# Kernel optimization log

Hardware: AMD Instinct MI355X
Metric: run time of the kernel (lower is better)

Reference implementation:

```python
import jax, jax.numpy as jnp
import numpy as np

H, DH = 16, 64          # num_heads, dim_head
DIM = 1024              # dim_ltn
EPS = 1e-5


def setup_inputs() -> dict:
    key = jax.random.key(0)
    ks = jax.random.split(key, 8)
    b, n_txt, t, m = 2, 2048, 4, 256
    text = jax.random.normal(ks[0], (b, n_txt, DIM), dtype=jnp.float32)
    image = jax.random.normal(ks[1], (b, t, m, DIM), dtype=jnp.float32)
    locations = jax.random.randint(ks[2], (b, n_txt), 0, 2)  # 0/1 media markers
    s = DIM ** -0.5
    Wq = jax.random.normal(ks[3], (DIM, H * DH), dtype=jnp.float32) * s
    Wkv = jax.random.normal(ks[4], (DIM, 2 * H * DH), dtype=jnp.float32) * s
    Wo = jax.random.normal(ks[5], (H * DH, DIM), dtype=jnp.float32) * s
    ln_gamma = jnp.ones((DIM,), dtype=jnp.float32)
    ln_beta = jnp.zeros((DIM,), dtype=jnp.float32)
    return {"text": text, "image": image, "locations": locations,
            "Wq": Wq, "Wkv": Wkv, "Wo": Wo,
            "ln_gamma": ln_gamma, "ln_beta": ln_beta}


def reference(text, image, locations, Wq, Wkv, Wo, ln_gamma, ln_beta):
    scale = DH ** -0.5
    b, t, m, d = image.shape
    # LayerNorm(text)
    mu = text.mean(-1, keepdims=True)
    var = ((text - mu) ** 2).mean(-1, keepdims=True)
    tn = (text - mu) / jnp.sqrt(var + EPS) * ln_gamma + ln_beta
    img = image.reshape(b, t * m, d)             # b (t m) d
    q = tn @ Wq                                  # b n (h dh)
    k, v = jnp.split(img @ Wkv, 2, axis=-1)      # each b tm (h dh)
    split_heads = lambda x: x.reshape(x.shape[0], x.shape[1], H, DH).transpose(0, 2, 1, 3)
    q, k, v = split_heads(q), split_heads(k), split_heads(v)
    attn = jnp.einsum('bhid,bhjd->bhij', q, k) * scale   # b h n (t m)
    txt_time = jnp.cumsum(locations, axis=-1)            # b n : media index per text token
    viz_time = jnp.repeat(jnp.arange(1, t + 1), m)       # (t m)
    # only_attend_to_immediate -> equality mask
    mask = txt_time[:, None, :, None] == viz_time[None, None, None, :]
    neg = -jnp.finfo(attn.dtype).max
    attn = jnp.where(mask, attn, neg)
    attn = jax.nn.softmax(attn, axis=-1)
    # zero attention for text tokens before any media (txt_time == 0)
    attn = jnp.where((txt_time == 0)[:, None, :, None], 0.0, attn)
    out = jnp.einsum('bhij,bhjd->bhid', attn, v)
    out = out.transpose(0, 2, 1, 3).reshape(b, -1, H * DH)
    return out @ Wo
```

## Files before the change

kernel.cpp:

```cpp
#include <hip/hip_runtime.h>

#define BATCH 2
#define NTXT  2048
#define TMED  4
#define MMED  256
#define TM    (TMED * MMED)
#define DIM   1024
#define NH    16
#define DHD   64
#define KVW   2048
#define RMAX  256
#define QSTR  ((size_t)BATCH * RMAX * DIM)

typedef _Float16 f16x8 __attribute__((ext_vector_type(8)));
typedef float    f32x4 __attribute__((ext_vector_type(4)));

__global__ __launch_bounds__(256) void k1_prep(
    const int* __restrict__ loc, const float* __restrict__ Wkv,
    int* __restrict__ tt, int* __restrict__ seg, float* __restrict__ vbar,
    _Float16* __restrict__ WkvT) {
  __shared__ float tile[64][65];
  __shared__ int tots[256];
  __shared__ int s_start, s_end;
  const int bid = blockIdx.x;
  const int tid = threadIdx.x;
  if (bid < BATCH) {
    const int b = bid;
    if (tid == 0) { s_start = NTXT; s_end = NTXT; }
    __syncthreads();
    int v[8];
    int run = 0;
    const int base = b * NTXT + tid * 8;
#pragma unroll
    for (int k = 0; k < 8; k++) { run += loc[base + k]; v[k] = run; }
    tots[tid] = run; __syncthreads();
    for (int off = 1; off < 256; off <<= 1) {
      const int add = (tid >= off) ? tots[tid - off] : 0;
      __syncthreads();
      tots[tid] += add;
      __syncthreads();
    }
    const int excl = tots[tid] - run;
#pragma unroll
    for (int k = 0; k < 8; k++) {
      const int tv = excl + v[k];
      tt[base + k] = tv;
      if (tv >= 1) atomicMin(&s_start, tid * 8 + k);
      if (tv >= 5) atomicMin(&s_end, tid * 8 + k);
    }
    __syncthreads();
    if (tid == 0) {
      seg[b * 2]     = s_start;
      seg[b * 2 + 1] = s_end - s_start;
    }
  } else if (bid == 2) {
    for (int c = tid; c < 2 * BATCH * DIM; c += 256) vbar[c] = 0.f;
  } else {
    const int idx = bid - 3;
    const int k0 = (idx & 15) * 64, n0 = (idx >> 4) * 64;
    const int r = tid >> 4, c4 = (tid & 15) * 4;
#pragma unroll
    for (int i = 0; i < 4; i++) {
      const float4 v = *reinterpret_cast<const float4*>(
          Wkv + (size_t)(k0 + r + i * 16) * KVW + n0 + c4);
      tile[r + i * 16][c4 + 0] = v.x; tile[r + i * 16][c4 + 1] = v.y;
      tile[r + i * 16][c4 + 2] = v.z; tile[r + i * 16][c4 + 3] = v.w;
    }
    __syncthreads();
#pragma unroll
    for (int it = 0; it < 2; it++) {
      const int chunk = it * 256 + tid;
      const int n = chunk >> 3, kc = (chunk & 7) * 8;
      f16x8 h;
#pragma unroll
      for (int j = 0; j < 8; j++) h[j] = (_Float16)tile[kc + j][n];
      *reinterpret_cast<f16x8*>(WkvT + (size_t)(n0 + n) * DIM + k0 + kc) = h;
    }
  }
}

__global__ __launch_bounds__(256) void k2_gemm_qproj(
    const float* __restrict__ image, const _Float16* __restrict__ WkvT,
    const float* __restrict__ text, const float* __restrict__ Wq,
    const float* __restrict__ gamma, const float* __restrict__ beta,
    const int* __restrict__ seg, _Float16* __restrict__ kv16,
    float* __restrict__ qpart, float* __restrict__ vbar) {
  __shared__ char smem[8192];
  const int idx = blockIdx.x;
  const int tid = threadIdx.x;
  if (idx >= 64) {
    _Float16* As = (_Float16*)smem;
    _Float16* Bs = As + 64 * 32;
    const int gid = idx - 64;
    const int lane = tid & 63, wid = tid >> 6;
    const int wm = wid & 1, wn = wid >> 1;
    const int row0 = (gid >> 5) * 64, col0 = (gid & 31) * 64;
    const int srow = tid >> 2, skc = (tid & 3) * 8;
    const int frow = lane & 15, fq = lane >> 4;
    f32x4 acc[2][2] = {};
    for (int k0 = 0; k0 < DIM; k0 += 32) {
      const float* ap = image + (size_t)(row0 + srow) * DIM + k0 + skc;
      const float4 a0 = *reinterpret_cast<const float4*>(ap);
      const float4 a1 = *reinterpret_cast<const float4*>(ap + 4);
      f16x8 av;
      av[0] = (_Float16)a0.x; av[1] = (_Float16)a0.y;
      av[2] = (_Float16)a0.z; av[3] = (_Float16)a0.w;
      av[4] = (_Float16)a1.x; av[5] = (_Float16)a1.y;
      av[6] = (_Float16)a1.z; av[7] = (_Float16)a1.w;
      const f16x8 bv = *reinterpret_cast<const f16x8*>(
          WkvT + (size_t)(col0 + srow) * DIM + k0 + skc);
      __syncthreads();
      *reinterpret_cast<f16x8*>(As + tid * 8) = av;
      *reinterpret_cast<f16x8*>(Bs + tid * 8) = bv;
      __syncthreads();
      f16x8 af[2], bf[2];
#pragma unroll
      for (int mt = 0; mt < 2; mt++)
        af[mt] = *reinterpret_cast<const f16x8*>(
            As + (wm * 32 + mt * 16 + frow) * 32 + fq * 8);
#pragma unroll
      for (int nt = 0; nt < 2; nt++)
        bf[nt] = *reinterpret_cast<const f16x8*>(
            Bs + (wn * 32 + nt * 16 + frow) * 32 + fq * 8);
#pragma unroll
      for (int mt = 0; mt < 2; mt++)
#pragma unroll
        for (int nt = 0; nt < 2; nt++)
          acc[mt][nt] = __builtin_amdgcn_mfma_f32_16x16x32_f16(
              af[mt], bf[nt], acc[mt][nt], 0, 0, 0);
    }
#pragma unroll
    for (int mt = 0; mt < 2; mt++)
#pragma unroll
      for (int nt = 0; nt < 2; nt++) {
        const int col = col0 + wn * 32 + nt * 16 + frow;
#pragma unroll
        for (int r = 0; r < 4; r++) {
          const int row = row0 + wm * 32 + mt * 16 + fq * 4 + r;
          kv16[(size_t)row * KVW + col] = (_Float16)acc[mt][nt][r];
        }
      }
    if (col0 >= DIM) {
      const int b = row0 >> 10;
#pragma unroll
      for (int nt = 0; nt < 2; nt++) {
        float s = 0.f;
#pragma unroll
        for (int mt = 0; mt < 2; mt++)
#pragma unroll
          for (int r = 0; r < 4; r++) s += acc[mt][nt][r];
        s += __shfl_down(s, 32);
        s += __shfl_down(s, 16);
        if (lane < 16)
          atomicAdd(&vbar[b * DIM + (col0 - DIM) + wn * 32 + nt * 16 + lane],
                    s * (1.0f / (float)TM));
      }
    }
  } else {
    float* tn_s = (float*)smem;
    const int j = idx;
    const int b = j >> 5, nt = (j >> 2) & 7, cc = j & 3;
    const int n0 = nt * 128, c0 = cc * 256;
    const int lane = tid & 63, w = tid >> 6;
    const int n = tid & 127, rh = tid >> 7;
    const int i0 = seg[b * 2];
    const int cnt = min(seg[b * 2 + 1], RMAX);
    float* qp = qpart + (size_t)cc * QSTR;
    for (int r0 = 0; r0 < cnt; r0 += 4) {
      const int rows = min(4, cnt - r0);
      if (w < rows) {
        const float* xrow = text + (size_t)(b * NTXT + i0 + r0 + w) * DIM;
        float s = 0.f, sq = 0.f;
#pragma unroll
        for (int u = 0; u < 16; u++) {
          const float x = xrow[lane + 64 * u];
          s += x; sq += x * x;
        }
#pragma unroll
        for (int off = 32; off > 0; off >>= 1) {
          s += __shfl_xor(s, off);
          sq += __shfl_xor(sq, off);
        }
        const float mu = s * (1.0f / DIM);
        const float rstd = rsqrtf(sq * (1.0f / DIM) - mu * mu + 1e-5f);
#pragma unroll
        for (int u = 0; u < 4; u++) {
          const int c = c0 + lane + 64 * u;
          tn_s[w * 256 + lane + 64 * u] =
              (xrow[c] - mu) * rstd * gamma[c] + beta[c];
        }
      }
      __syncthreads();
      float a0 = 0.f, a1 = 0.f;
      for (int c = 0; c < 256; c++) {
        const float wv = Wq[(size_t)(c0 + c) * DIM + n0 + n];
        a0 += tn_s[(rh * 2) * 256 + c] * wv;
        a1 += tn_s[(rh * 2 + 1) * 256 + c] * wv;
      }
      if (rh * 2 < rows)
        qp[(size_t)(b * RMAX + r0 + rh * 2) * DIM + n0 + n] = a0;
      if (rh * 2 + 1 < rows)
        qp[(size_t)(b * RMAX + r0 + rh * 2 + 1) * DIM + n0 + n] = a1;
      __syncthreads();
    }
  }
}

__global__ __launch_bounds__(512) void k3_obar(
    const float* __restrict__ vbar, const float* __restrict__ Wo,
    float* __restrict__ obar) {
  __shared__ float vb_s[128];
  const int bid = blockIdx.x;
  const int tid = threadIdx.x;
  const int b = bid >> 4, et = (bid >> 3) & 1, cc = bid & 7;
  const int e = et * 512 + tid, c0 = cc * 128;
  if (tid < 128) vb_s[tid] = vbar[b * DIM + c0 + tid];
  __syncthreads();
  float s = 0.f;
  for (int c = 0; c < 128; c++)
    s += vb_s[c] * Wo[(size_t)(c0 + c) * DIM + e];
  atomicAdd(&obar[b * DIM + e], s);
}

__global__ __launch_bounds__(256) void k4_fill_attn(
    const float* __restrict__ text, const _Float16* __restrict__ kv16,
    const float* __restrict__ Wq, const float* __restrict__ Wo,
    const float* __restrict__ gamma, const float* __restrict__ beta,
    const int* __restrict__ tt, const int* __restrict__ seg,
    const float* __restrict__ obar, const float* __restrict__ qpart,
    float* __restrict__ oacc, float* __restrict__ out) {
  __shared__ float red[256];
  __shared__ float pbuf[256];
  const int idx = blockIdx.x;
  const int tid = threadIdx.x;
  if (idx < BATCH * NTXT) {
    const int b = idx >> 11;
    const int i = idx & (NTXT - 1);
    const int t = tt[idx];
    float* orow = out + (size_t)idx * DIM;
    if (t == 0) {
      *reinterpret_cast<float4*>(&orow[tid * 4]) =
          make_float4(0.f, 0.f, 0.f, 0.f);
      return;
    }
    if (t > TMED) {
      *reinterpret_cast<float4*>(&orow[tid * 4]) =
          *reinterpret_cast<const float4*>(&obar[b * DIM + tid * 4]);
      return;
    }
    if (i - seg[b * 2] < RMAX) return;
    __shared__ float tns[DIM];
    __shared__ float qrow[DIM];
    __shared__ float oaccs[DIM];
    const float* xrow = text + (size_t)idx * DIM;
    float x[4];
    float s = 0.f;
#pragma unroll
    for (int u = 0; u < 4; u++) { x[u] = xrow[tid + 256 * u]; s += x[u]; }
    red[tid] = s; __syncthreads();
    for (int st = 128; st > 0; st >>= 1) {
      if (tid < st) red[tid] += red[tid + st];
      __syncthreads();
    }
    const float mu = red[0] * (1.0f / DIM); __syncthreads();
    float vs = 0.f;
#pragma unroll
    for (int u = 0; u < 4; u++) { float d = x[u] - mu; vs += d * d; }
    red[tid] = vs; __syncthreads();
    for (int st = 128; st > 0; st >>= 1) {
      if (tid < st) red[tid] += red[tid + st];
      __syncthreads();
    }
    const float rstd = rsqrtf(red[0] * (1.0f / DIM) + 1e-5f); __syncthreads();
#pragma unroll
    for (int u = 0; u < 4; u++) {
      const int c = tid + 256 * u;
      tns[c] = (x[u] - mu) * rstd * gamma[c] + beta[c];
    }
    __syncthreads();
    {
      float qa[4] = {0.f, 0.f, 0.f, 0.f};
      for (int c = 0; c < DIM; c++) {
        const float tv = tns[c];
        const float* wp = Wq + (size_t)c * DIM + tid;
#pragma unroll
        for (int u = 0; u < 4; u++) qa[u] += tv * wp[256 * u];
      }
#pragma unroll
      for (int u = 0; u < 4; u++) qrow[tid + 256 * u] = qa[u];
    }
    __syncthreads();
    const size_t kvrow0 = (size_t)(b * TM + (t - 1) * MMED) * KVW;
    const int d0 = tid & 63, g = tid >> 6;
    for (int h = 0; h < NH; h++) {
      const _Float16* krow = kv16 + kvrow0 + (size_t)tid * KVW + h * DHD;
      float sc = 0.f;
#pragma unroll
      for (int d = 0; d < DHD; d++) sc += qrow[h * DHD + d] * (float)krow[d];
      sc *= 0.125f;
      red[tid] = sc; __syncthreads();
      for (int st = 128; st > 0; st >>= 1) {
        if (tid < st) red[tid] = fmaxf(red[tid], red[tid + st]);
        __syncthreads();
      }
      const float mx = red[0]; __syncthreads();
      const float e = __expf(sc - mx);
      red[tid] = e; __syncthreads();
      for (int st = 128; st > 0; st >>= 1) {
        if (tid < st) red[tid] += red[tid + st];
        __syncthreads();
      }
      const float inv = 1.0f / red[0]; __syncthreads();
      pbuf[tid] = e * inv; __syncthreads();
      const _Float16* vbase =
          kv16 + kvrow0 + (size_t)(g * 64) * KVW + DIM + h * DHD + d0;
      float a = 0.f;
#pragma unroll 8
      for (int jj = 0; jj < 64; jj++)
        a += pbuf[g * 64 + jj] * (float)vbase[(size_t)jj * KVW];
      red[tid] = a; __syncthreads();
      if (tid < 64)
        oaccs[h * DHD + tid] =
            red[tid] + red[64 + tid] + red[128 + tid] + red[192 + tid];
      __syncthreads();
    }
    float oa[4] = {0.f, 0.f, 0.f, 0.f};
    for (int c = 0; c < DIM; c++) {
      const float ov = oaccs[c];
      const float* wp = Wo + (size_t)c * DIM + tid;
#pragma unroll
      for (int u = 0; u < 4; u++) oa[u] += ov * wp[256 * u];
    }
#pragma unroll
    for (int u = 0; u < 4; u++) orow[tid + 256 * u] = oa[u];
  } else {
    __shared__ float qs[DHD];
    const int j = idx - BATCH * NTXT;
    const int h = j & 15, rt = (j >> 4) & 31, b = j >> 9;
    const int i0 = seg[b * 2];
    const int cnt = min(seg[b * 2 + 1], RMAX);
    const int d0 = tid & 63, g = tid >> 6;
    for (int r = rt; r < cnt; r += 32) {
      const int i = i0 + r;
      const int t = tt[b * NTXT + i];
      if (tid < 64) {
        const size_t qoff = (size_t)(b * RMAX + r) * DIM + h * DHD + tid;
        qs[tid] = qpart[qoff] + qpart[QSTR + qoff] +
                  qpart[2 * QSTR + qoff] + qpart[3 * QSTR + qoff];
      }
      __syncthreads();
      const size_t kvrow0 = (size_t)(b * TM + (t - 1) * MMED) * KVW;
      const _Float16* krow = kv16 + kvrow0 + (size_t)tid * KVW + h * DHD;
      float sc = 0.f;
#pragma unroll
      for (int d = 0; d < DHD; d += 8) {
        const f16x8 kk = *reinterpret_cast<const f16x8*>(krow + d);
#pragma unroll
        for (int u = 0; u < 8; u++) sc += qs[d + u] * (float)kk[u];
      }
      sc *= 0.125f;
      red[tid] = sc; __syncthreads();
      for (int st = 128; st > 0; st >>= 1) {
        if (tid < st) red[tid] = fmaxf(red[tid], red[tid + st]);
        __syncthreads();
      }
      const float mx = red[0]; __syncthreads();
      const float e = __expf(sc - mx);
      red[tid] = e; __syncthreads();
      for (int st = 128; st > 0; st >>= 1) {
        if (tid < st) red[tid] += red[tid + st];
        __syncthreads();
      }
      const float inv = 1.0f / red[0]; __syncthreads();
      pbuf[tid] = e * inv; __syncthreads();
      const _Float16* vbase =
          kv16 + kvrow0 + (size_t)(g * 64) * KVW + DIM + h * DHD + d0;
      float a = 0.f;
#pragma unroll 8
      for (int jj = 0; jj < 64; jj++)
        a += pbuf[g * 64 + jj] * (float)vbase[(size_t)jj * KVW];
      red[tid] = a; __syncthreads();
      if (tid < 64)
        oacc[(size_t)(b * RMAX + r) * DIM + h * DHD + tid] =
            red[tid] + red[64 + tid] + red[128 + tid] + red[192 + tid];
      __syncthreads();
    }
  }
}

__global__ __launch_bounds__(256) void k5_oproj(
    const float* __restrict__ oacc, const float* __restrict__ Wo,
    const int* __restrict__ seg, float* __restrict__ out) {
  const int ct = blockIdx.x;
  const int rt = blockIdx.y;
  const int b = blockIdx.z;
  const int i0 = seg[b * 2];
  const int cnt = min(seg[b * 2 + 1], RMAX);
  const int tid = threadIdx.x;
  const int d0 = tid & 63, g = tid >> 6;
  __shared__ float op[4][64];
  for (int r = rt; r < cnt; r += 32) {
    const float* arow = oacc + (size_t)(b * RMAX + r) * DIM;
    const float* wo = Wo + (size_t)(g * 256) * DIM + ct * 64 + d0;
    float s = 0.f;
    for (int c = 0; c < 256; c++) s += arow[g * 256 + c] * wo[(size_t)c * DIM];
    op[g][d0] = s; __syncthreads();
    if (tid < 64)
      out[(size_t)(b * NTXT + i0 + r) * DIM + ct * 64 + tid] =
          op[0][tid] + op[1][tid] + op[2][tid] + op[3][tid];
    __syncthreads();
  }
}

extern "C" void kernel_launch(void* const* d_in, const int* in_sizes, int n_in,
                              void* d_out, int out_size, void* d_ws, size_t ws_size,
                              hipStream_t stream) {
  const float* text  = (const float*)d_in[0];
  const float* image = (const float*)d_in[1];
  const int*   loc   = (const int*)d_in[2];
  const float* Wq    = (const float*)d_in[3];
  const float* Wkv   = (const float*)d_in[4];
  const float* Wo    = (const float*)d_in[5];
  const float* gamma = (const float*)d_in[6];
  const float* beta  = (const float*)d_in[7];
  float* out = (float*)d_out;

  _Float16* kv16  = (_Float16*)d_ws;
  _Float16* WkvT  = kv16 + (size_t)BATCH * TM * KVW;
  float*    oacc  = (float*)WkvT;
  float*    qpart = (float*)(WkvT + (size_t)KVW * DIM);
  float*    vbar  = qpart + 4 * QSTR;
  float*    obar  = vbar + BATCH * DIM;
  int*      tt    = (int*)(obar + BATCH * DIM);
  int*      seg   = tt + BATCH * NTXT;

  k1_prep<<<515, 256, 0, stream>>>(loc, Wkv, tt, seg, vbar, WkvT);
  k2_gemm_qproj<<<1088, 256, 0, stream>>>(image, WkvT, text, Wq, gamma, beta,
                                          seg, kv16, qpart, vbar);
  k3_obar<<<32, 512, 0, stream>>>(vbar, Wo, obar);
  k4_fill_attn<<<BATCH * NTXT + NH * 32 * BATCH, 256, 0, stream>>>(
      text, kv16, Wq, Wo, gamma, beta, tt, seg, obar, qpart, oacc, out);
  k5_oproj<<<dim3(16, 32, BATCH), 256, 0, stream>>>(oacc, Wo, seg, out);
}
```

Before: 187.2 us.

## Compute vbar from image mean, enlarge KV GEMM tile, restage attention and oproj

The mean of V is now computed algebraically as mean(image) @ Wv in the prep kernel, written as deterministic partial sums instead of atomics from the GEMM epilogue. The obar projection moves into the GEMM kernel as partials. The KV GEMM tile grows from 64 to 128 rows per block, which halves the number of blocks and reuses each B tile across more rows. Attention moves into its own kernel together with the obar reduction, and the output projection runs alongside the fill kernel, which removes one launch. The cost is extra partial-buffer traffic, and the fp32 mean path differs numerically from the previous f16 accumulation.

```diff
diff --git a/kernel.cpp b/kernel.cpp
--- a/kernel.cpp
+++ b/kernel.cpp
@@ -11,14 +11,16 @@
 #define KVW   2048
 #define RMAX  256
 #define QSTR  ((size_t)BATCH * RMAX * DIM)
+#define BD    (BATCH * DIM)
 
 typedef _Float16 f16x8 __attribute__((ext_vector_type(8)));
 typedef float    f32x4 __attribute__((ext_vector_type(4)));
 
 __global__ __launch_bounds__(256) void k1_prep(
     const int* __restrict__ loc, const float* __restrict__ Wkv,
-    int* __restrict__ tt, int* __restrict__ seg, float* __restrict__ vbar,
-    _Float16* __restrict__ WkvT) {
+    const float* __restrict__ image, int* __restrict__ tt,
+    int* __restrict__ seg, _Float16* __restrict__ WkvT,
+    float* __restrict__ vpart) {
   __shared__ float tile[64][65];
   __shared__ int tots[256];
   __shared__ int s_start, s_end;
@@ -53,10 +55,37 @@
       seg[b * 2]     = s_start;
       seg[b * 2 + 1] = s_end - s_start;
     }
-  } else if (bid == 2) {
-    for (int c = tid; c < 2 * BATCH * DIM; c += 256) vbar[c] = 0.f;
+  } else if (bid < 66) {
+    float* part = (float*)tile;
+    const int j = bid - 2;
+    const int b = j >> 5, cc = j & 31;
+    const int c0 = cc * 32;
+    const int c = tid & 31, jg = tid >> 5;
+    const float* p = image + (size_t)(b * TM + jg * 128) * DIM + c0 + c;
+    float s = 0.f;
+#pragma unroll 4
+    for (int j2 = 0; j2 < 128; j2++) s += p[(size_t)j2 * DIM];
+    part[jg * 32 + c] = s;
+    __syncthreads();
+    if (tid < 32) {
+      float t2 = 0.f;
+#pragma unroll
+      for (int g = 0; g < 8; g++) t2 += part[g * 32 + tid];
+      part[tid] = t2 * (1.0f / (float)TM);
+    }
+    __syncthreads();
+    float a4[4] = {};
+    for (int c2 = 0; c2 < 32; c2++) {
+      const float ib = part[c2];
+      const float* wrow = Wkv + (size_t)(c0 + c2) * KVW + DIM + tid;
+#pragma unroll
+      for (int u = 0; u < 4; u++) a4[u] += ib * wrow[u * 256];
+    }
+#pragma unroll
+    for (int u = 0; u < 4; u++)
+      vpart[(size_t)cc * BD + b * DIM + tid + u * 256] = a4[u];
   } else {
-    const int idx = bid - 3;
+    const int idx = bid - 66;
     const int k0 = (idx & 15) * 64, n0 = (idx >> 4) * 64;
     const int r = tid >> 4, c4 = (tid & 15) * 4;
 #pragma unroll
@@ -79,84 +108,17 @@
   }
 }
 
-__global__ __launch_bounds__(256) void k2_gemm_qproj(
+__global__ __launch_bounds__(256) void k2_gemm_qproj_opart(
     const float* __restrict__ image, const _Float16* __restrict__ WkvT,
     const float* __restrict__ text, const float* __restrict__ Wq,
-    const float* __restrict__ gamma, const float* __restrict__ beta,
-    const int* __restrict__ seg, _Float16* __restrict__ kv16,
-    float* __restrict__ qpart, float* __restrict__ vbar) {
-  __shared__ char smem[8192];
+    const float* __restrict__ Wo, const float* __restrict__ gamma,
+    const float* __restrict__ beta, const int* __restrict__ seg,
+    const float* __restrict__ vpart, _Float16* __restrict__ kv16,
+    float* __restrict__ qpart, float* __restrict__ opart) {
+  __shared__ char smem[12288];
   const int idx = blockIdx.x;
   const int tid = threadIdx.x;
-  if (idx >= 64) {
-    _Float16* As = (_Float16*)smem;
-    _Float16* Bs = As + 64 * 32;
-    const int gid = idx - 64;
-    const int lane = tid & 63, wid = tid >> 6;
-    const int wm = wid & 1, wn = wid >> 1;
-    const int row0 = (gid >> 5) * 64, col0 = (gid & 31) * 64;
-    const int srow = tid >> 2, skc = (tid & 3) * 8;
-    const int frow = lane & 15, fq = lane >> 4;
-    f32x4 acc[2][2] = {};
-    for (int k0 = 0; k0 < DIM; k0 += 32) {
-      const float* ap = image + (size_t)(row0 + srow) * DIM + k0 + skc;
-      const float4 a0 = *reinterpret_cast<const float4*>(ap);
-      const float4 a1 = *reinterpret_cast<const float4*>(ap + 4);
-      f16x8 av;
-      av[0] = (_Float16)a0.x; av[1] = (_Float16)a0.y;
-      av[2] = (_Float16)a0.z; av[3] = (_Float16)a0.w;
-      av[4] = (_Float16)a1.x; av[5] = (_Float16)a1.y;
-      av[6] = (_Float16)a1.z; av[7] = (_Float16)a1.w;
-      const f16x8 bv = *reinterpret_cast<const f16x8*>(
-          WkvT + (size_t)(col0 + srow) * DIM + k0 + skc);
-      __syncthreads();
-      *reinterpret_cast<f16x8*>(As + tid * 8) = av;
-      *reinterpret_cast<f16x8*>(Bs + tid * 8) = bv;
-      __syncthreads();
-      f16x8 af[2], bf[2];
-#pragma unroll
-      for (int mt = 0; mt < 2; mt++)
-        af[mt] = *reinterpret_cast<const f16x8*>(
-            As + (wm * 32 + mt * 16 + frow) * 32 + fq * 8);
-#pragma unroll
-      for (int nt = 0; nt < 2; nt++)
-        bf[nt] = *reinterpret_cast<const f16x8*>(
-            Bs + (wn * 32 + nt * 16 + frow) * 32 + fq * 8);
-#pragma unroll
-      for (int mt = 0; mt < 2; mt++)
-#pragma unroll
-        for (int nt = 0; nt < 2; nt++)
-          acc[mt][nt] = __builtin_amdgcn_mfma_f32_16x16x32_f16(
-              af[mt], bf[nt], acc[mt][nt], 0, 0, 0);
-    }
-#pragma unroll
-    for (int mt = 0; mt < 2; mt++)
-#pragma unroll
-      for (int nt = 0; nt < 2; nt++) {
-        const int col = col0 + wn * 32 + nt * 16 + frow;
-#pragma unroll
-        for (int r = 0; r < 4; r++) {
-          const int row = row0 + wm * 32 + mt * 16 + fq * 4 + r;
-          kv16[(size_t)row * KVW + col] = (_Float16)acc[mt][nt][r];
-        }
-      }
-    if (col0 >= DIM) {
-      const int b = row0 >> 10;
-#pragma unroll
-      for (int nt = 0; nt < 2; nt++) {
-        float s = 0.f;
-#pragma unroll
-        for (int mt = 0; mt < 2; mt++)
-#pragma unroll
-          for (int r = 0; r < 4; r++) s += acc[mt][nt][r];
-        s += __shfl_down(s, 32);
-        s += __shfl_down(s, 16);
-        if (lane < 16)
-          atomicAdd(&vbar[b * DIM + (col0 - DIM) + wn * 32 + nt * 16 + lane],
-                    s * (1.0f / (float)TM));
-      }
-    }
-  } else {
+  if (idx < 64) {
     float* tn_s = (float*)smem;
     const int j = idx;
     const int b = j >> 5, nt = (j >> 2) & 7, cc = j & 3;
@@ -203,32 +165,167 @@
         qp[(size_t)(b * RMAX + r0 + rh * 2 + 1) * DIM + n0 + n] = a1;
       __syncthreads();
     }
+  } else if (idx < 80) {
+    float* vb_s = (float*)smem;
+    const int j = idx - 64;
+    const int b = j >> 3, cc = j & 7;
+    const int e0 = cc * 128;
+    if (tid < 128) {
+      float s = 0.f;
+#pragma unroll 8
+      for (int ch = 0; ch < 32; ch++)
+        s += vpart[(size_t)ch * BD + b * DIM + e0 + tid];
+      vb_s[tid] = s;
+    }
+    __syncthreads();
+    float a4[4] = {};
+    for (int c = 0; c < 128; c++) {
+      const float vv = vb_s[c];
+      const float* wrow = Wo + (size_t)(e0 + c) * DIM + tid;
+#pragma unroll
+      for (int u = 0; u < 4; u++) a4[u] += vv * wrow[u * 256];
+    }
+#pragma unroll
+    for (int u = 0; u < 4; u++)
+      opart[(size_t)cc * BD + b * DIM + tid + u * 256] = a4[u];
+  } else {
+    _Float16* As = (_Float16*)smem;
+    _Float16* Bs = As + 128 * 32;
+    const int gid = idx - 80;
+    const int lane = tid & 63, wid = tid >> 6;
+    const int wm = wid & 1, wn = wid >> 1;
+    const int row0 = (gid >> 5) * 128, col0 = (gid & 31) * 64;
+    const int ar = tid >> 2, ak = (tid & 3) * 8;
+    const int frow = lane & 15, fq = lane >> 4;
+    f32x4 acc[4][2] = {};
+    for (int k0 = 0; k0 < DIM; k0 += 32) {
+      f16x8 av[2];
+#pragma unroll
+      for (int s2 = 0; s2 < 2; s2++) {
+        const float* ap =
+            image + (size_t)(row0 + ar + s2 * 64) * DIM + k0 + ak;
+        const float4 a0 = *reinterpret_cast<const float4*>(ap);
+        const float4 a1 = *reinterpret_cast<const float4*>(ap + 4);
+        av[s2][0] = (_Float16)a0.x; av[s2][1] = (_Float16)a0.y;
+        av[s2][2] = (_Float16)a0.z; av[s2][3] = (_Float16)a0.w;
+        av[s2][4] = (_Float16)a1.x; av[s2][5] = (_Float16)a1.y;
+        av[s2][6] = (_Float16)a1.z; av[s2][7] = (_Float16)a1.w;
+      }
+      const f16x8 bv = *reinterpret_cast<const f16x8*>(
+          WkvT + (size_t)(col0 + ar) * DIM + k0 + ak);
+      __syncthreads();
+      *reinterpret_cast<f16x8*>(As + ar * 32 + ak) = av[0];
+      *reinterpret_cast<f16x8*>(As + (ar + 64) * 32 + ak) = av[1];
+      *reinterpret_cast<f16x8*>(Bs + ar * 32 + ak) = bv;
+      __syncthreads();
+      f16x8 af[4], bf[2];
+#pragma unroll
+      for (int mt = 0; mt < 4; mt++)
+        af[mt] = *reinterpret_cast<const f16x8*>(
+            As + (wm * 64 + mt * 16 + frow) * 32 + fq * 8);
+#pragma unroll
+      for (int nt = 0; nt < 2; nt++)
+        bf[nt] = *reinterpret_cast<const f16x8*>(
+            Bs + (wn * 32 + nt * 16 + frow) * 32 + fq * 8);
+#pragma unroll
+      for (int mt = 0; mt < 4; mt++)
+#pragma unroll
+        for (int nt = 0; nt < 2; nt++)
+          acc[mt][nt] = __builtin_amdgcn_mfma_f32_16x16x32_f16(
+              af[mt], bf[nt], acc[mt][nt], 0, 0, 0);
+    }
+#pragma unroll
+    for (int mt = 0; mt < 4; mt++)
+#pragma unroll
+      for (int nt = 0; nt < 2; nt++) {
+        const int col = col0 + wn * 32 + nt * 16 + frow;
+#pragma unroll
+        for (int r = 0; r < 4; r++) {
+          const int row = row0 + wm * 64 + mt * 16 + fq * 4 + r;
+          kv16[(size_t)row * KVW + col] = (_Float16)acc[mt][nt][r];
+        }
+      }
   }
 }
 
-__global__ __launch_bounds__(512) void k3_obar(
-    const float* __restrict__ vbar, const float* __restrict__ Wo,
+__global__ __launch_bounds__(256) void k3_attn_obar(
+    const _Float16* __restrict__ kv16, const int* __restrict__ tt,
+    const int* __restrict__ seg, const float* __restrict__ qpart,
+    const float* __restrict__ opart, float* __restrict__ oacc,
     float* __restrict__ obar) {
-  __shared__ float vb_s[128];
-  const int bid = blockIdx.x;
+  __shared__ float red[256];
+  __shared__ float pbuf[256];
+  __shared__ float qs[DHD];
+  const int idx = blockIdx.x;
   const int tid = threadIdx.x;
-  const int b = bid >> 4, et = (bid >> 3) & 1, cc = bid & 7;
-  const int e = et * 512 + tid, c0 = cc * 128;
-  if (tid < 128) vb_s[tid] = vbar[b * DIM + c0 + tid];
-  __syncthreads();
-  float s = 0.f;
-  for (int c = 0; c < 128; c++)
-    s += vb_s[c] * Wo[(size_t)(c0 + c) * DIM + e];
-  atomicAdd(&obar[b * DIM + e], s);
+  if (idx >= 1024) {
+    const int b = idx - 1024;
+    for (int e = tid; e < DIM; e += 256) {
+      float s = 0.f;
+#pragma unroll
+      for (int cc = 0; cc < 8; cc++) s += opart[(size_t)cc * BD + b * DIM + e];
+      obar[b * DIM + e] = s;
+    }
+    return;
+  }
+  const int h = idx & 15, rt = (idx >> 4) & 31, b = idx >> 9;
+  const int i0 = seg[b * 2];
+  const int cnt = min(seg[b * 2 + 1], RMAX);
+  const int d0 = tid & 63, g = tid >> 6;
+  for (int r = rt; r < cnt; r += 32) {
+    const int i = i0 + r;
+    const int t = tt[b * NTXT + i];
+    if (tid < 64) {
+      const size_t qoff = (size_t)(b * RMAX + r) * DIM + h * DHD + tid;
+      qs[tid] = qpart[qoff] + qpart[QSTR + qoff] +
+                qpart[2 * QSTR + qoff] + qpart[3 * QSTR + qoff];
+    }
+    __syncthreads();
+    const size_t kvrow0 = (size_t)(b * TM + (t - 1) * MMED) * KVW;
+    const _Float16* krow = kv16 + kvrow0 + (size_t)tid * KVW + h * DHD;
+    float sc = 0.f;
+#pragma unroll
+    for (int d = 0; d < DHD; d += 8) {
+      const f16x8 kk = *reinterpret_cast<const f16x8*>(krow + d);
+#pragma unroll
+      for (int u = 0; u < 8; u++) sc += qs[d + u] * (float)kk[u];
+    }
+    sc *= 0.125f;
+    red[tid] = sc; __syncthreads();
+    for (int st = 128; st > 0; st >>= 1) {
+      if (tid < st) red[tid] = fmaxf(red[tid], red[tid + st]);
+      __syncthreads();
+    }
+    const float mx = red[0]; __syncthreads();
+    const float e = __expf(sc - mx);
+    red[tid] = e; __syncthreads();
+    for (int st = 128; st > 0; st >>= 1) {
+      if (tid < st) red[tid] += red[tid + st];
+      __syncthreads();
+    }
+    const float inv = 1.0f / red[0]; __syncthreads();
+    pbuf[tid] = e * inv; __syncthreads();
+    const _Float16* vbase =
+        kv16 + kvrow0 + (size_t)(g * 64) * KVW + DIM + h * DHD + d0;
+    float a = 0.f;
+#pragma unroll 8
+    for (int jj = 0; jj < 64; jj++)
+      a += pbuf[g * 64 + jj] * (float)vbase[(size_t)jj * KVW];
+    red[tid] = a; __syncthreads();
+    if (tid < 64)
+      oacc[(size_t)(b * RMAX + r) * DIM + h * DHD + tid] =
+          red[tid] + red[64 + tid] + red[128 + tid] + red[192 + tid];
+    __syncthreads();
+  }
 }
 
-__global__ __launch_bounds__(256) void k4_fill_attn(
+__global__ __launch_bounds__(256) void k4_fill_oproj(
     const float* __restrict__ text, const _Float16* __restrict__ kv16,
     const float* __restrict__ Wq, const float* __restrict__ Wo,
     const float* __restrict__ gamma, const float* __restrict__ beta,
     const int* __restrict__ tt, const int* __restrict__ seg,
-    const float* __restrict__ obar, const float* __restrict__ qpart,
-    float* __restrict__ oacc, float* __restrict__ out) {
+    const float* __restrict__ obar, const float* __restrict__ oacc,
+    float* __restrict__ out) {
   __shared__ float red[256];
   __shared__ float pbuf[256];
   const int idx = blockIdx.x;
@@ -334,81 +431,24 @@
 #pragma unroll
     for (int u = 0; u < 4; u++) orow[tid + 256 * u] = oa[u];
   } else {
-    __shared__ float qs[DHD];
+    __shared__ float op[4][64];
     const int j = idx - BATCH * NTXT;
-    const int h = j & 15, rt = (j >> 4) & 31, b = j >> 9;
+    const int ct = j & 15, rt = (j >> 4) & 31, b = j >> 9;
     const int i0 = seg[b * 2];
     const int cnt = min(seg[b * 2 + 1], RMAX);
     const int d0 = tid & 63, g = tid >> 6;
     for (int r = rt; r < cnt; r += 32) {
-      const int i = i0 + r;
-      const int t = tt[b * NTXT + i];
-      if (tid < 64) {
-        const size_t qoff = (size_t)(b * RMAX + r) * DIM + h * DHD + tid;
-        qs[tid] = qpart[qoff] + qpart[QSTR + qoff] +
-                  qpart[2 * QSTR + qoff] + qpart[3 * QSTR + qoff];
-      }
-      __syncthreads();
-      const size_t kvrow0 = (size_t)(b * TM + (t - 1) * MMED) * KVW;
-      const _Float16* krow = kv16 + kvrow0 + (size_t)tid * KVW + h * DHD;
-      float sc = 0.f;
-#pragma unroll
-      for (int d = 0; d < DHD; d += 8) {
-        const f16x8 kk = *reinterpret_cast<const f16x8*>(krow + d);
-#pragma unroll
-        for (int u = 0; u < 8; u++) sc += qs[d + u] * (float)kk[u];
-      }
-      sc *= 0.125f;
-      red[tid] = sc; __syncthreads();
-      for (int st = 128; st > 0; st >>= 1) {
-        if (tid < st) red[tid] = fmaxf(red[tid], red[tid + st]);
-        __syncthreads();
-      }
-      const float mx = red[0]; __syncthreads();
-      const float e = __expf(sc - mx);
-      red[tid] = e; __syncthreads();
-      for (int st = 128; st > 0; st >>= 1) {
-        if (tid < st) red[tid] += red[tid + st];
-        __syncthreads();
-      }
-      const float inv = 1.0f / red[0]; __syncthreads();
-      pbuf[tid] = e * inv; __syncthreads();
-      const _Float16* vbase =
-          kv16 + kvrow0 + (size_t)(g * 64) * KVW + DIM + h * DHD + d0;
-      float a = 0.f;
-#pragma unroll 8
-      for (int jj = 0; jj < 64; jj++)
-        a += pbuf[g * 64 + jj] * (float)vbase[(size_t)jj * KVW];
-      red[tid] = a; __syncthreads();
+      const float* arow = oacc + (size_t)(b * RMAX + r) * DIM;
+      const float* wo = Wo + (size_t)(g * 256) * DIM + ct * 64 + d0;
+      float s = 0.f;
+      for (int c = 0; c < 256; c++)
+        s += arow[g * 256 + c] * wo[(size_t)c * DIM];
+      op[g][d0] = s; __syncthreads();
       if (tid < 64)
-        oacc[(size_t)(b * RMAX + r) * DIM + h * DHD + tid] =
-            red[tid] + red[64 + tid] + red[128 + tid] + red[192 + tid];
-      __syncthreads();
-    }
-  }
-}
-
-__global__ __launch_bounds__(256) void k5_oproj(
-    const float* __restrict__ oacc, const float* __restrict__ Wo,
-    const int* __restrict__ seg, float* __restrict__ out) {
-  const int ct = blockIdx.x;
-  const int rt = blockIdx.y;
-  const int b = blockIdx.z;
-  const int i0 = seg[b * 2];
-  const int cnt = min(seg[b * 2 + 1], RMAX);
-  const int tid = threadIdx.x;
-  const int d0 = tid & 63, g = tid >> 6;
-  __shared__ float op[4][64];
-  for (int r = rt; r < cnt; r += 32) {
-    const float* arow = oacc + (size_t)(b * RMAX + r) * DIM;
-    const float* wo = Wo + (size_t)(g * 256) * DIM + ct * 64 + d0;
-    float s = 0.f;
-    for (int c = 0; c < 256; c++) s += arow[g * 256 + c] * wo[(size_t)c * DIM];
-    op[g][d0] = s; __syncthreads();
-    if (tid < 64)
-      out[(size_t)(b * NTXT + i0 + r) * DIM + ct * 64 + tid] =
-          op[0][tid] + op[1][tid] + op[2][tid] + op[3][tid];
-    __syncthreads();
+        out[(size_t)(b * NTXT + i0 + r) * DIM + ct * 64 + tid] =
+            op[0][tid] + op[1][tid] + op[2][tid] + op[3][tid];
+      __syncthreads();
+    }
   }
 }
 
@@ -429,16 +469,18 @@
   _Float16* WkvT  = kv16 + (size_t)BATCH * TM * KVW;
   float*    oacc  = (float*)WkvT;
   float*    qpart = (float*)(WkvT + (size_t)KVW * DIM);
-  float*    vbar  = qpart + 4 * QSTR;
-  float*    obar  = vbar + BATCH * DIM;
-  int*      tt    = (int*)(obar + BATCH * DIM);
+  float*    vpart = qpart + 4 * QSTR;
+  float*    opart = vpart + 32 * BD;
+  float*    obar  = opart + 8 * BD;
+  int*      tt    = (int*)(obar + BD);
   int*      seg   = tt + BATCH * NTXT;
 
-  k1_prep<<<515, 256, 0, stream>>>(loc, Wkv, tt, seg, vbar, WkvT);
-  k2_gemm_qproj<<<1088, 256, 0, stream>>>(image, WkvT, text, Wq, gamma, beta,
-                                          seg, kv16, qpart, vbar);
-  k3_obar<<<32, 512, 0, stream>>>(vbar, Wo, obar);
-  k4_fill_attn<<<BATCH * NTXT + NH * 32 * BATCH, 256, 0, stream>>>(
-      text, kv16, Wq, Wo, gamma, beta, tt, seg, obar, qpart, oacc, out);
-  k5_oproj<<<dim3(16, 32, BATCH), 256, 0, stream>>>(oacc, Wo, seg, out);
+  k1_prep<<<578, 256, 0, stream>>>(loc, Wkv, image, tt, seg, WkvT, vpart);
+  k2_gemm_qproj_opart<<<592, 256, 0, stream>>>(image, WkvT, text, Wq, Wo,
+                                               gamma, beta, seg, vpart, kv16,
+                                               qpart, opart);
+  k3_attn_obar<<<1026, 256, 0, stream>>>(kv16, tt, seg, qpart, opart, oacc,
+                                         obar);
+  k4_fill_oproj<<<BATCH * NTXT + 1024, 256, 0, stream>>>(
+      text, kv16, Wq, Wo, gamma, beta, tt, seg, obar, oacc, out);
 }
```

After: 178.6 us. -4.6%, faster.
